# Optimization experiments

Measured on AMD Instinct MI355X. Metric: run time of the kernel, lower is better.

Reference implementation:

```python
import jax, jax.numpy as jnp
import numpy as np

EMBED_DIM = 512
N_HEADS = 8
HEAD_DIM = EMBED_DIM // N_HEADS
N_BINS = 512
MAX_BIN = 256
SCALE = 1.0 / np.sqrt(HEAD_DIM)


def _l2norm(x):
    # manifold.project onto unit sphere along last dim
    n = jnp.sqrt(jnp.sum(x * x, axis=-1, keepdims=True))
    return x / jnp.maximum(n, 1e-12)


def setup_inputs() -> dict:
    rng = jax.random.key(0)
    ks = jax.random.split(rng, 13)
    B, N, D = 1, 2048, EMBED_DIM
    s = 1.0 / np.sqrt(D)
    cen = jax.random.normal(ks[12], (N_BINS, HEAD_DIM), dtype=jnp.float32)
    return {
        "query": jax.random.normal(ks[0], (B, N, D), dtype=jnp.float32),
        "key": jax.random.normal(ks[1], (B, N, D), dtype=jnp.float32),
        "value": jax.random.normal(ks[2], (B, N, D), dtype=jnp.float32),
        "Wq": jax.random.normal(ks[3], (D, D), dtype=jnp.float32) * s,
        "bq": jax.random.normal(ks[4], (D,), dtype=jnp.float32) * s,
        "Wk": jax.random.normal(ks[5], (D, D), dtype=jnp.float32) * s,
        "bk": jax.random.normal(ks[6], (D,), dtype=jnp.float32) * s,
        "Wv": jax.random.normal(ks[7], (D, D), dtype=jnp.float32) * s,
        "bv": jax.random.normal(ks[8], (D,), dtype=jnp.float32) * s,
        "Wo": jax.random.normal(ks[9], (D, D), dtype=jnp.float32) * s,
        "bo": jax.random.normal(ks[10], (D,), dtype=jnp.float32) * s,
        "centroids": _l2norm(cen),  # unit bin centroids of dim head_dim
    }


def reference(query, key, value, Wq, bq, Wk, bk, Wv, bv, Wo, bo, centroids):
    B, Nq, D = query.shape
    Nk = key.shape[1]
    H, hd = N_HEADS, HEAD_DIM

    def split(x):  # [B,N,D] -> [B,H,N,hd]
        return x.reshape(B, -1, H, hd).transpose(0, 2, 1, 3)

    q = split(query @ Wq.T + bq)
    k = split(key @ Wk.T + bk)
    v = split(value @ Wv.T + bv)

    # manifold.project (sphere): attention uses the projected q/k, raw v
    qn = _l2norm(q)
    kn = _l2norm(k)

    # DavisCache: nearest-centroid bin id  [B,H,N]
    qb = jnp.argmax(jnp.einsum('bhnd,cd->bhnc', qn, centroids), axis=-1).astype(jnp.int32)
    kb = jnp.argmax(jnp.einsum('bhnd,cd->bhnc', kn, centroids), axis=-1).astype(jnp.int32)

    # neighboring_bins(qb, radius=1) on a ring: kb in {qb-1, qb, qb+1} mod N_BINS
    diff = (qb[..., :, None] - kb[..., None, :]) % N_BINS  # [B,H,Nq,Nk]
    neigh = (diff <= 1) | (diff >= N_BINS - 1)

    # truncate to first MAX_BIN selected keys (index order), as in the loop
    rank = jnp.cumsum(neigh.astype(jnp.int32), axis=-1)  # inclusive count
    sel = neigh & (rank <= MAX_BIN)
    # fallback: empty neighbor set -> all keys, then truncated to first MAX_BIN
    fallback = (jnp.arange(Nk, dtype=jnp.int32) < MAX_BIN)
    mask = jnp.where(neigh.any(axis=-1, keepdims=True), sel, fallback)

    scores = jnp.einsum('bhqd,bhkd->bhqk', qn, kn) * jnp.float32(SCALE)
    scores = jnp.where(mask, scores, jnp.float32(-1e30))
    attn = jax.nn.softmax(scores, axis=-1)  # dropout=0.0 (eval)
    out = jnp.einsum('bhqk,bhkd->bhqd', attn, v)

    out = out.transpose(0, 2, 1, 3).reshape(B, Nq, D)
    return out @ Wo.T + bo
```

## Files before the change

### kernel.cpp

```cpp
#include <hip/hip_runtime.h>
#include <hip/hip_bf16.h>

#define NTOK 2048
#define EMBED 512
#define NHEADS 8
#define HD 64
#define NBINS 512
#define MAXSEL 256

typedef unsigned short u16;
typedef unsigned int u32;

__device__ __forceinline__ float lof(u32 u){ return __uint_as_float(u << 16); }
__device__ __forceinline__ float hif(u32 u){ return __uint_as_float(u & 0xffff0000u); }
__device__ __forceinline__ float bf2f(u16 u){ return __uint_as_float(((u32)u) << 16); }
__device__ __forceinline__ u16 f2b(float f){
    __hip_bfloat16 h = __float2bfloat16(f);
    return *(u16*)&h;
}
__device__ __forceinline__ u32 pack2(float lo, float hi){
    return (u32)f2b(lo) | ((u32)f2b(hi) << 16);
}
__device__ __forceinline__ void fma8(const float* x, u32 ux, u32 uy, u32 uz, u32 uw, float& a){
    a += x[0]*lof(ux) + x[1]*hif(ux) + x[2]*lof(uy) + x[3]*hif(uy)
       + x[4]*lof(uz) + x[5]*hif(uz) + x[6]*lof(uw) + x[7]*hif(uw);
}

__device__ __forceinline__ u32 sniffp(const void* p){
    const u16* s = (const u16*)p;
    float m = 0.f;
    #pragma unroll
    for (int k=0; k<64; k++) m = fmaxf(m, fabsf(bf2f(s[2*k])));
    return (m > 100.f) ? 1u : 0u;
}

__device__ __forceinline__ void ub2(const uint4& u, float4& f0, float4& f1){
    f0 = make_float4(lof(u.x), hif(u.x), lof(u.y), hif(u.y));
    f1 = make_float4(lof(u.z), hif(u.z), lof(u.w), hif(u.w));
}

__device__ __forceinline__ void fma16x2(const float* xp,
    const float4& a0, const float4& a1, const float4& a2, const float4& a3,
    const float4& b0, const float4& b1, const float4& b2, const float4& b3,
    float& A, float& B)
{
    float4 x0 = *(const float4*)(xp);
    float4 x1 = *(const float4*)(xp+4);
    float4 x2 = *(const float4*)(xp+8);
    float4 x3 = *(const float4*)(xp+12);
    A += x0.x*a0.x; A += x0.y*a0.y; A += x0.z*a0.z; A += x0.w*a0.w;
    A += x1.x*a1.x; A += x1.y*a1.y; A += x1.z*a1.z; A += x1.w*a1.w;
    A += x2.x*a2.x; A += x2.y*a2.y; A += x2.z*a2.z; A += x2.w*a2.w;
    A += x3.x*a3.x; A += x3.y*a3.y; A += x3.z*a3.z; A += x3.w*a3.w;
    B += x0.x*b0.x; B += x0.y*b0.y; B += x0.z*b0.z; B += x0.w*b0.w;
    B += x1.x*b1.x; B += x1.y*b1.y; B += x1.z*b1.z; B += x1.w*b1.w;
    B += x2.x*b2.x; B += x2.y*b2.y; B += x2.z*b2.z; B += x2.w*b2.w;
    B += x3.x*b3.x; B += x3.y*b3.y; B += x3.z*b3.z; B += x3.w*b3.w;
}

__global__ __launch_bounds__(256) void projqkv_kernel(
    const void* __restrict__ Xq, const void* __restrict__ Xk, const void* __restrict__ Xv,
    const void* __restrict__ Wq, const void* __restrict__ bq,
    const void* __restrict__ Wk, const void* __restrict__ bk,
    const void* __restrict__ Wv, const void* __restrict__ bv,
    const void* __restrict__ cen,
    void* __restrict__ outQ,
    u16* __restrict__ Kb, u16* __restrict__ Vb,
    u16* __restrict__ qbin, u16* __restrict__ kbin)
{
    int which = blockIdx.y;
    const void *X, *W, *Bb;
    if (which==0){ X=Xq; W=Wq; Bb=bq; }
    else if (which==1){ X=Xk; W=Wk; Bb=bk; }
    else { X=Xv; W=Wv; Bb=bv; }
    u32 fx = sniffp(X), fw = sniffp(W), fb = sniffp(Bb);
    int r0 = blockIdx.x * 8;
    int t = threadIdx.x;

    __shared__ __align__(16) float ubuf[4608];
    __shared__ __align__(16) float ps[64*68];
    __shared__ float nrm2[64][4];
    __shared__ float invn[64];
    __shared__ float bvl[64][8];
    __shared__ int   bil[64][8];

    float* xstage = ps;
    for (int i=t; i<1024; i+=256){
        int row = i>>7, c4 = i&127;
        float4 v;
        if (!fx){
            const u32* xp = (const u32*)((const u16*)X + (size_t)(r0+row)*EMBED);
            u32 a = xp[c4*2], b = xp[c4*2+1];
            v = make_float4(lof(a), hif(a), lof(b), hif(b));
        } else {
            v = ((const float4*)((const float*)X + (size_t)(r0+row)*EMBED))[c4];
        }
        *(float4*)(xstage + row*516 + c4*4) = v;
    }
    __syncthreads();

    float acc2[8][2];
    #pragma unroll
    for (int r=0;r<8;r++){ acc2[r][0]=0.f; acc2[r][1]=0.f; }

    if (fw){
        const float* w1 = (const float*)W + (size_t)t*EMBED;
        const float* w2 = (const float*)W + (size_t)(t+256)*EMBED;
        float4 pa0 = *(const float4*)(w1+ 0), pa1 = *(const float4*)(w1+ 4),
               pa2 = *(const float4*)(w1+ 8), pa3 = *(const float4*)(w1+12);
        float4 pb0 = *(const float4*)(w2+ 0), pb1 = *(const float4*)(w2+ 4),
               pb2 = *(const float4*)(w2+ 8), pb3 = *(const float4*)(w2+12);
        #pragma unroll 1
        for (int k0=0; k0<512; k0+=32){
            float4 qa0 = *(const float4*)(w1+k0+16), qa1 = *(const float4*)(w1+k0+20),
                   qa2 = *(const float4*)(w1+k0+24), qa3 = *(const float4*)(w1+k0+28);
            float4 qb0 = *(const float4*)(w2+k0+16), qb1 = *(const float4*)(w2+k0+20),
                   qb2 = *(const float4*)(w2+k0+24), qb3 = *(const float4*)(w2+k0+28);
            #pragma unroll
            for (int r=0;r<8;r++)
                fma16x2(xstage + r*516 + k0, pa0,pa1,pa2,pa3, pb0,pb1,pb2,pb3,
                        acc2[r][0], acc2[r][1]);
            if (k0+32 < 512){
                pa0 = *(const float4*)(w1+k0+32); pa1 = *(const float4*)(w1+k0+36);
                pa2 = *(const float4*)(w1+k0+40); pa3 = *(const float4*)(w1+k0+44);
                pb0 = *(const float4*)(w2+k0+32); pb1 = *(const float4*)(w2+k0+36);
                pb2 = *(const float4*)(w2+k0+40); pb3 = *(const float4*)(w2+k0+44);
            }
            #pragma unroll
            for (int r=0;r<8;r++)
                fma16x2(xstage + r*516 + k0+16, qa0,qa1,qa2,qa3, qb0,qb1,qb2,qb3,
                        acc2[r][0], acc2[r][1]);
        }
    } else {
        const uint4* w1 = (const uint4*)((const u16*)W + (size_t)t*EMBED);
        const uint4* w2 = (const uint4*)((const u16*)W + (size_t)(t+256)*EMBED);
        uint4 pa0 = w1[0], pa1 = w1[1], pb0 = w2[0], pb1 = w2[1];
        #pragma unroll 1
        for (int k0=0; k0<512; k0+=32){
            int u = k0>>3;
            uint4 qa0 = w1[u+2], qa1 = w1[u+3], qb0 = w2[u+2], qb1 = w2[u+3];
            float4 a0,a1,a2,a3,b0,b1,b2,b3;
            ub2(pa0,a0,a1); ub2(pa1,a2,a3); ub2(pb0,b0,b1); ub2(pb1,b2,b3);
            #pragma unroll
            for (int r=0;r<8;r++)
                fma16x2(xstage + r*516 + k0, a0,a1,a2,a3, b0,b1,b2,b3,
                        acc2[r][0], acc2[r][1]);
            if (k0+32 < 512){ pa0 = w1[u+4]; pa1 = w1[u+5]; pb0 = w2[u+4]; pb1 = w2[u+5]; }
            ub2(qa0,a0,a1); ub2(qa1,a2,a3); ub2(qb0,b0,b1); ub2(qb1,b2,b3);
            #pragma unroll
            for (int r=0;r<8;r++)
                fma16x2(xstage + r*516 + k0+16, a0,a1,a2,a3, b0,b1,b2,b3,
                        acc2[r][0], acc2[r][1]);
        }
    }
    __syncthreads();
    {
        float b0 = fb ? ((const float*)Bb)[t]     : bf2f(((const u16*)Bb)[t]);
        float b1 = fb ? ((const float*)Bb)[t+256] : bf2f(((const u16*)Bb)[t+256]);
        int h0 = t>>6, c0 = t&63, h1 = (t+256)>>6, c1 = (t+256)&63;
        #pragma unroll
        for (int r=0;r<8;r++){
            ps[(r*8+h0)*68 + c0] = acc2[r][0]+b0;
            ps[(r*8+h1)*68 + c1] = acc2[r][1]+b1;
        }
    }
    __syncthreads();

    if (which == 2){
        int hr = t>>2, q4 = t&3;
        int row = hr>>3, head = hr&7;
        const float* src = ps + hr*68 + q4*16;
        u16* dst = Vb + (size_t)(r0+row)*EMBED + head*64 + q4*16;
        #pragma unroll
        for (int j8=0;j8<2;j8++){
            uint4 v;
            v.x = pack2(src[j8*8+0],src[j8*8+1]); v.y = pack2(src[j8*8+2],src[j8*8+3]);
            v.z = pack2(src[j8*8+4],src[j8*8+5]); v.w = pack2(src[j8*8+6],src[j8*8+7]);
            ((uint4*)dst)[j8] = v;
        }
        return;
    }

    u32 fc = sniffp(cen);
    int rg = t>>3, cg = t&7;
    float best[2] = {-3.4e38f,-3.4e38f};
    int   bidx[2] = {0,0};
    float cpre[16];
    #pragma unroll
    for (int it=0; it<16; it++){
        int e = t + it*256, j = e>>6, k = e&63;
        cpre[it] = fc ? ((const float*)cen)[(size_t)j*HD + k]
                      : bf2f(((const u16*)cen)[(size_t)j*HD + k]);
    }
    for (int tt=0; tt<8; tt++){
        __syncthreads();
        #pragma unroll
        for (int it=0; it<16; it++){
            int e = t + it*256, j = e>>6, k = e&63;
            ubuf[k*68 + j] = cpre[it];
        }
        if (tt < 7){
            #pragma unroll
            for (int it=0; it<16; it++){
                int e = t + it*256, j = e>>6, k = e&63;
                int gj = (tt+1)*64 + j;
                cpre[it] = fc ? ((const float*)cen)[(size_t)gj*HD + k]
                              : bf2f(((const u16*)cen)[(size_t)gj*HD + k]);
            }
        }
        __syncthreads();
        float acc[2][8];
        #pragma unroll
        for (int j=0;j<2;j++)
            #pragma unroll
            for (int c=0;c<8;c++) acc[j][c]=0.f;
        const float* pr0 = ps + (2*rg)*68;
        const float* pr1 = pr0 + 68;
        #pragma unroll 1
        for (int k4=0;k4<64;k4+=4){
            float4 ra = *(const float4*)(pr0 + k4);
            float4 rb = *(const float4*)(pr1 + k4);
            const float* cbase = ubuf + k4*68 + cg*8;
            #define SCANK(OFF, AX, BX) { \
                const float4* cp = (const float4*)(cbase + (OFF)); \
                float4 c0 = cp[0], c1 = cp[1]; \
                acc[0][0]+=(AX)*c0.x; acc[0][1]+=(AX)*c0.y; acc[0][2]+=(AX)*c0.z; acc[0][3]+=(AX)*c0.w; \
                acc[0][4]+=(AX)*c1.x; acc[0][5]+=(AX)*c1.y; acc[0][6]+=(AX)*c1.z; acc[0][7]+=(AX)*c1.w; \
                acc[1][0]+=(BX)*c0.x; acc[1][1]+=(BX)*c0.y; acc[1][2]+=(BX)*c0.z; acc[1][3]+=(BX)*c0.w; \
                acc[1][4]+=(BX)*c1.x; acc[1][5]+=(BX)*c1.y; acc[1][6]+=(BX)*c1.z; acc[1][7]+=(BX)*c1.w; }
            SCANK(0,   ra.x, rb.x)
            SCANK(68,  ra.y, rb.y)
            SCANK(136, ra.z, rb.z)
            SCANK(204, ra.w, rb.w)
            #undef SCANK
        }
        #pragma unroll
        for (int j=0;j<2;j++){
            #pragma unroll
            for (int c=0;c<8;c++){
                int gi = tt*64 + cg*8 + c;
                if (acc[j][c] > best[j]){ best[j]=acc[j][c]; bidx[j]=gi; }
            }
        }
    }
    bvl[2*rg  ][cg]=best[0]; bil[2*rg  ][cg]=bidx[0];
    bvl[2*rg+1][cg]=best[1]; bil[2*rg+1][cg]=bidx[1];
    {
        int hr = t>>2, q4 = t&3;
        const float* src = ps + hr*68 + q4*16;
        float ss=0.f;
        #pragma unroll
        for (int d=0;d<16;d++) ss += src[d]*src[d];
        nrm2[hr][q4]=ss;
    }
    __syncthreads();
    if (t < 64){
        int hr = t;
        invn[hr] = 1.f / fmaxf(sqrtf(nrm2[hr][0]+nrm2[hr][1]+nrm2[hr][2]+nrm2[hr][3]), 1e-12f);
        float bv = bvl[hr][0]; int bi = bil[hr][0];
        #pragma unroll
        for (int g=1; g<8; g++){
            float ov = bvl[hr][g]; int oi = bil[hr][g];
            if (ov > bv || (ov == bv && oi < bi)){ bv = ov; bi = oi; }
        }
        u16* bins = (which==0) ? qbin : kbin;
        int token = r0 + (hr>>3), head = hr&7;
        bins[head*NTOK + token] = (u16)bi;
    }
    __syncthreads();
    {
        int hr = t>>2, q4 = t&3;
        float inv = invn[hr];
        const float* src = ps + hr*68 + q4*16;
        int row = hr>>3, head = hr&7;
        size_t off = (size_t)(r0+row)*EMBED + head*64 + q4*16;
        if (which == 1){
            u16* dst = Kb + off;
            #pragma unroll
            for (int j8=0;j8<2;j8++){
                uint4 v;
                v.x = pack2(src[j8*8+0]*inv, src[j8*8+1]*inv);
                v.y = pack2(src[j8*8+2]*inv, src[j8*8+3]*inv);
                v.z = pack2(src[j8*8+4]*inv, src[j8*8+5]*inv);
                v.w = pack2(src[j8*8+6]*inv, src[j8*8+7]*inv);
                ((uint4*)dst)[j8] = v;
            }
        } else if (!fx){
            u16* dst = (u16*)outQ + off;
            #pragma unroll
            for (int j8=0;j8<2;j8++){
                uint4 v;
                v.x = pack2(src[j8*8+0]*inv, src[j8*8+1]*inv);
                v.y = pack2(src[j8*8+2]*inv, src[j8*8+3]*inv);
                v.z = pack2(src[j8*8+4]*inv, src[j8*8+5]*inv);
                v.w = pack2(src[j8*8+6]*inv, src[j8*8+7]*inv);
                ((uint4*)dst)[j8] = v;
            }
        } else {
            float* dst = (float*)outQ + off;
            #pragma unroll
            for (int j4=0;j4<4;j4++){
                float4 v = make_float4(src[j4*4+0]*inv, src[j4*4+1]*inv,
                                       src[j4*4+2]*inv, src[j4*4+3]*inv);
                ((float4*)dst)[j4] = v;
            }
        }
    }
}

__global__ __launch_bounds__(256) void attn_kernel(
    const void* __restrict__ query,
    const u16* __restrict__ Kb, const u16* __restrict__ Vb,
    const u16* __restrict__ qbin, const u16* __restrict__ kbin,
    void* __restrict__ out)
{
    u32 fq = sniffp(query);
    int q = blockIdx.x, t = threadIdx.x;
    int wave = t>>6, lane = t&63;
    __shared__ float qs[512];
    __shared__ float sc[4][256];
    __shared__ u16   sel[4][256];

    if (!fq){
        u32 u = ((const u32*)out)[(size_t)q*256 + t];
        qs[2*t] = lof(u); qs[2*t+1] = hif(u);
    } else {
        float2 f = ((const float2*)out)[(size_t)q*256 + t];
        qs[2*t] = f.x; qs[2*t+1] = f.y;
    }
    __syncthreads();

    for (int hh=0; hh<2; hh++){
        int h = wave*2 + hh;
        int myqb = qbin[h*NTOK + q];
        const uint4* kbp = (const uint4*)(kbin + h*NTOK + lane*32);
        u32 fl = 0;
        #pragma unroll
        for (int w4=0; w4<4; w4++){
            uint4 kw = kbp[w4];
            u32 arr[4] = {kw.x, kw.y, kw.z, kw.w};
            #pragma unroll
            for (int e=0;e<4;e++){
                int b0 = (int)(arr[e] & 0xffff), b1 = (int)(arr[e] >> 16);
                int d0 = (myqb - b0) & (NBINS-1), d1 = (myqb - b1) & (NBINS-1);
                if (d0 <= 1 || d0 >= NBINS-1) fl |= 1u << (w4*8 + e*2);
                if (d1 <= 1 || d1 >= NBINS-1) fl |= 1u << (w4*8 + e*2 + 1);
            }
        }
        int cnt = __popc(fl);
        int sum = cnt;
        #pragma unroll
        for (int off=1; off<64; off<<=1){
            int v = __shfl_up(sum, off, 64);
            if (lane >= off) sum += v;
        }
        int total = __shfl(sum, 63, 64);
        int r = sum - cnt;
        if (total){
            u32 f2 = fl;
            while (f2){
                int j = __ffs(f2) - 1; f2 &= f2 - 1;
                if (r < MAXSEL) sel[wave][r] = (u16)(lane*32 + j);
                r++;
            }
        } else {
            #pragma unroll
            for (int kq=0;kq<4;kq++) sel[wave][lane*4+kq] = (u16)(lane*4+kq);
        }
        int L = total ? min(total, MAXSEL) : MAXSEL;
        __asm__ volatile("s_waitcnt lgkmcnt(0)" ::: "memory");
        const float* qh = qs + h*64;

        if (L <= 64){
            int kkey = 0;
            float s = -3.4e38f;
            if (lane < L){
                kkey = sel[wave][lane];
                const uint4* kr = (const uint4*)(Kb + (size_t)kkey*EMBED + h*64);
                float acc = 0.f;
                #pragma unroll
                for (int p=0;p<8;p++){ uint4 u = kr[p]; fma8(qh+p*8, u.x,u.y,u.z,u.w, acc); }
                s = acc * 0.125f;
            }
            float mloc = s;
            #pragma unroll
            for (int off=32; off; off>>=1) mloc = fmaxf(mloc, __shfl_xor(mloc, off, 64));
            float e = (lane < L) ? __expf(s - mloc) : 0.f;
            float ssum = e;
            #pragma unroll
            for (int off=32; off; off>>=1) ssum += __shfl_xor(ssum, off, 64);
            float inv = 1.f / fmaxf(ssum, 1e-37f);
            const u16* vb = Vb + h*64 + lane;
            float acc = 0.f;
            int j = 0;
            for (; j+4<=L; j+=4){
                float e0 = __shfl(e, j,   64), e1 = __shfl(e, j+1, 64);
                float e2 = __shfl(e, j+2, 64), e3 = __shfl(e, j+3, 64);
                int   k0 = __shfl(kkey, j,   64), k1 = __shfl(kkey, j+1, 64);
                int   k2 = __shfl(kkey, j+2, 64), k3 = __shfl(kkey, j+3, 64);
                float v0 = bf2f(vb[(size_t)k0*EMBED]);
                float v1 = bf2f(vb[(size_t)k1*EMBED]);
                float v2 = bf2f(vb[(size_t)k2*EMBED]);
                float v3 = bf2f(vb[(size_t)k3*EMBED]);
                acc += e0*v0; acc += e1*v1; acc += e2*v2; acc += e3*v3;
            }
            for (; j<L; j++){
                float ej = __shfl(e, j, 64);
                int   kj = __shfl(kkey, j, 64);
                acc += ej * bf2f(vb[(size_t)kj*EMBED]);
            }
            float o = acc * inv;
            if (!fq) ((u16*)out)[(size_t)q*EMBED + h*64 + lane] = f2b(o);
            else     ((float*)out)[(size_t)q*EMBED + h*64 + lane] = o;
        } else {
            float mloc = -3.4e38f;
            for (int jj=lane; jj<L; jj+=64){
                int kkey = sel[wave][jj];
                const uint4* kr = (const uint4*)(Kb + (size_t)kkey*EMBED + h*64);
                float acc = 0.f;
                #pragma unroll
                for (int p=0;p<8;p++){ uint4 u = kr[p]; fma8(qh+p*8, u.x,u.y,u.z,u.w, acc); }
                float s = acc * 0.125f;
                sc[wave][jj] = s;
                mloc = fmaxf(mloc, s);
            }
            #pragma unroll
            for (int off=32; off; off>>=1) mloc = fmaxf(mloc, __shfl_xor(mloc, off, 64));
            float ssum = 0.f;
            for (int jj=lane; jj<L; jj+=64){
                float e = __expf(sc[wave][jj] - mloc);
                sc[wave][jj] = e; ssum += e;
            }
            #pragma unroll
            for (int off=32; off; off>>=1) ssum += __shfl_xor(ssum, off, 64);
            float inv = 1.f / fmaxf(ssum, 1e-37f);
            __asm__ volatile("s_waitcnt lgkmcnt(0)" ::: "memory");
            float acc = 0.f;
            for (int j=0; j<L; j++){
                int kkey = sel[wave][j];
                acc += sc[wave][j] * bf2f(Vb[(size_t)kkey*EMBED + h*64 + lane]);
            }
            float o = acc * inv;
            if (!fq) ((u16*)out)[(size_t)q*EMBED + h*64 + lane] = f2b(o);
            else     ((float*)out)[(size_t)q*EMBED + h*64 + lane] = o;
        }
    }
}

__global__ __launch_bounds__(256) void oproj_kernel(
    void* __restrict__ out, const void* __restrict__ Wo, const void* __restrict__ bo)
{
    u32 fq = sniffp(out);
    u32 fw = sniffp(Wo), fb = sniffp(bo);
    int r0 = blockIdx.x * 8;
    int t = threadIdx.x;
    __shared__ __align__(16) float xst[8*516];

    for (int i=t; i<1024; i+=256){
        int row = i>>7, c4 = i&127;
        float4 v;
        if (!fq){
            const u32* xp = (const u32*)((const u16*)out + (size_t)(r0+row)*EMBED);
            u32 a = xp[c4*2], b = xp[c4*2+1];
            v = make_float4(lof(a), hif(a), lof(b), hif(b));
        } else {
            v = ((const float4*)((const float*)out + (size_t)(r0+row)*EMBED))[c4];
        }
        *(float4*)(xst + row*516 + c4*4) = v;
    }
    __syncthreads();

    float acc2[8][2];
    #pragma unroll
    for (int r=0;r<8;r++){ acc2[r][0]=0.f; acc2[r][1]=0.f; }

    if (fw){
        const float* w1 = (const float*)Wo + (size_t)t*EMBED;
        const float* w2 = (const float*)Wo + (size_t)(t+256)*EMBED;
        float4 pa0 = *(const float4*)(w1+ 0), pa1 = *(const float4*)(w1+ 4),
               pa2 = *(const float4*)(w1+ 8), pa3 = *(const float4*)(w1+12);
        float4 pb0 = *(const float4*)(w2+ 0), pb1 = *(const float4*)(w2+ 4),
               pb2 = *(const float4*)(w2+ 8), pb3 = *(const float4*)(w2+12);
        #pragma unroll 1
        for (int k0=0; k0<512; k0+=32){
            float4 qa0 = *(const float4*)(w1+k0+16), qa1 = *(const float4*)(w1+k0+20),
                   qa2 = *(const float4*)(w1+k0+24), qa3 = *(const float4*)(w1+k0+28);
            float4 qb0 = *(const float4*)(w2+k0+16), qb1 = *(const float4*)(w2+k0+20),
                   qb2 = *(const float4*)(w2+k0+24), qb3 = *(const float4*)(w2+k0+28);
            #pragma unroll
            for (int r=0;r<8;r++)
                fma16x2(xst + r*516 + k0, pa0,pa1,pa2,pa3, pb0,pb1,pb2,pb3,
                        acc2[r][0], acc2[r][1]);
            if (k0+32 < 512){
                pa0 = *(const float4*)(w1+k0+32); pa1 = *(const float4*)(w1+k0+36);
                pa2 = *(const float4*)(w1+k0+40); pa3 = *(const float4*)(w1+k0+44);
                pb0 = *(const float4*)(w2+k0+32); pb1 = *(const float4*)(w2+k0+36);
                pb2 = *(const float4*)(w2+k0+40); pb3 = *(const float4*)(w2+k0+44);
            }
            #pragma unroll
            for (int r=0;r<8;r++)
                fma16x2(xst + r*516 + k0+16, qa0,qa1,qa2,qa3, qb0,qb1,qb2,qb3,
                        acc2[r][0], acc2[r][1]);
        }
    } else {
        const uint4* w1 = (const uint4*)((const u16*)Wo + (size_t)t*EMBED);
        const uint4* w2 = (const uint4*)((const u16*)Wo + (size_t)(t+256)*EMBED);
        uint4 pa0 = w1[0], pa1 = w1[1], pb0 = w2[0], pb1 = w2[1];
        #pragma unroll 1
        for (int k0=0; k0<512; k0+=32){
            int u = k0>>3;
            uint4 qa0 = w1[u+2], qa1 = w1[u+3], qb0 = w2[u+2], qb1 = w2[u+3];
            float4 a0,a1,a2,a3,b0,b1,b2,b3;
            ub2(pa0,a0,a1); ub2(pa1,a2,a3); ub2(pb0,b0,b1); ub2(pb1,b2,b3);
            #pragma unroll
            for (int r=0;r<8;r++)
                fma16x2(xst + r*516 + k0, a0,a1,a2,a3, b0,b1,b2,b3,
                        acc2[r][0], acc2[r][1]);
            if (k0+32 < 512){ pa0 = w1[u+4]; pa1 = w1[u+5]; pb0 = w2[u+4]; pb1 = w2[u+5]; }
            ub2(qa0,a0,a1); ub2(qa1,a2,a3); ub2(qb0,b0,b1); ub2(qb1,b2,b3);
            #pragma unroll
            for (int r=0;r<8;r++)
                fma16x2(xst + r*516 + k0+16, a0,a1,a2,a3, b0,b1,b2,b3,
                        acc2[r][0], acc2[r][1]);
        }
    }
    float b0 = fb ? ((const float*)bo)[t]     : bf2f(((const u16*)bo)[t]);
    float b1 = fb ? ((const float*)bo)[t+256] : bf2f(((const u16*)bo)[t+256]);
    if (!fq){
        u16* o = (u16*)out;
        #pragma unroll
        for (int r=0;r<8;r++){
            o[(size_t)(r0+r)*EMBED + t]       = f2b(acc2[r][0]+b0);
            o[(size_t)(r0+r)*EMBED + t + 256] = f2b(acc2[r][1]+b1);
        }
    } else {
        float* o = (float*)out;
        #pragma unroll
        for (int r=0;r<8;r++){
            o[(size_t)(r0+r)*EMBED + t]       = acc2[r][0]+b0;
            o[(size_t)(r0+r)*EMBED + t + 256] = acc2[r][1]+b1;
        }
    }
}

extern "C" void kernel_launch(void* const* d_in, const int* in_sizes, int n_in,
                              void* d_out, int out_size, void* d_ws, size_t ws_size,
                              hipStream_t stream)
{
    const void* query = d_in[0];
    const void* key   = d_in[1];
    const void* value = d_in[2];
    const void* Wq = d_in[3];
    const void* bq = d_in[4];
    const void* Wk = d_in[5];
    const void* bk = d_in[6];
    const void* Wv = d_in[7];
    const void* bv = d_in[8];
    const void* Wo = d_in[9];
    const void* bo = d_in[10];
    const void* cen = d_in[11];

    char* ws = (char*)d_ws;
    u16* qbin = (u16*)ws;
    u16* kbin = (u16*)(ws + 32768);
    u16* Kb   = (u16*)(ws + 65536);
    u16* Vb   = (u16*)(ws + 65536 + (size_t)2*1024*1024);

    projqkv_kernel<<<dim3(256,3), 256, 0, stream>>>(query,key,value,Wq,bq,Wk,bk,Wv,bv,cen,
                                                    d_out,Kb,Vb,qbin,kbin);
    attn_kernel<<<2048, 256, 0, stream>>>(query,Kb,Vb,qbin,kbin,d_out);
    oproj_kernel<<<256, 256, 0, stream>>>(d_out,Wo,bo);
}
```

Measured before the change: 277.7 us.

## Split K across thread halves so each thread accumulates four projection columns

The QKV projection GEMM is reorganised so that each thread computes four output columns over half of the K dimension, with the two halves of the block splitting K. The upper half writes its partial sums to a shared buffer, and the lower half adds them together with the bias. Each staged x vector read from LDS now feeds four weight rows instead of two, which cuts LDS traffic per FMA. The cost is an extra shared-memory reduction, a sync, and more accumulator registers.

```diff
diff --git a/kernel.cpp b/kernel.cpp
--- a/kernel.cpp
+++ b/kernel.cpp
@@ -37,6 +37,14 @@
 __device__ __forceinline__ void ub2(const uint4& u, float4& f0, float4& f1){
     f0 = make_float4(lof(u.x), hif(u.x), lof(u.y), hif(u.y));
     f1 = make_float4(lof(u.z), hif(u.z), lof(u.w), hif(u.w));
+}
+
+__device__ __forceinline__ float dot8(const float4& x0, const float4& x1,
+                                      const float4& a0, const float4& a1){
+    float s;
+    s  = x0.x*a0.x; s += x0.y*a0.y; s += x0.z*a0.z; s += x0.w*a0.w;
+    s += x1.x*a1.x; s += x1.y*a1.y; s += x1.z*a1.z; s += x1.w*a1.w;
+    return s;
 }
 
 __device__ __forceinline__ void fma16x2(const float* xp,
@@ -99,69 +107,98 @@
     }
     __syncthreads();
 
-    float acc2[8][2];
+    int tp = t & 127;
+    int kh = t >> 7;
+    int kbase = kh << 8;
+
+    float acc4[8][4];
     #pragma unroll
-    for (int r=0;r<8;r++){ acc2[r][0]=0.f; acc2[r][1]=0.f; }
+    for (int r=0;r<8;r++){ acc4[r][0]=0.f; acc4[r][1]=0.f; acc4[r][2]=0.f; acc4[r][3]=0.f; }
 
     if (fw){
-        const float* w1 = (const float*)W + (size_t)t*EMBED;
-        const float* w2 = (const float*)W + (size_t)(t+256)*EMBED;
-        float4 pa0 = *(const float4*)(w1+ 0), pa1 = *(const float4*)(w1+ 4),
-               pa2 = *(const float4*)(w1+ 8), pa3 = *(const float4*)(w1+12);
-        float4 pb0 = *(const float4*)(w2+ 0), pb1 = *(const float4*)(w2+ 4),
-               pb2 = *(const float4*)(w2+ 8), pb3 = *(const float4*)(w2+12);
+        const float* w0 = (const float*)W + (size_t)(tp      )*EMBED + kbase;
+        const float* w1 = (const float*)W + (size_t)(tp + 128)*EMBED + kbase;
+        const float* w2 = (const float*)W + (size_t)(tp + 256)*EMBED + kbase;
+        const float* w3 = (const float*)W + (size_t)(tp + 384)*EMBED + kbase;
+        float4 a00 = *(const float4*)(w0+0), a01 = *(const float4*)(w0+4);
+        float4 a10 = *(const float4*)(w1+0), a11 = *(const float4*)(w1+4);
+        float4 a20 = *(const float4*)(w2+0), a21 = *(const float4*)(w2+4);
+        float4 a30 = *(const float4*)(w3+0), a31 = *(const float4*)(w3+4);
         #pragma unroll 1
-        for (int k0=0; k0<512; k0+=32){
-            float4 qa0 = *(const float4*)(w1+k0+16), qa1 = *(const float4*)(w1+k0+20),
-                   qa2 = *(const float4*)(w1+k0+24), qa3 = *(const float4*)(w1+k0+28);
-            float4 qb0 = *(const float4*)(w2+k0+16), qb1 = *(const float4*)(w2+k0+20),
-                   qb2 = *(const float4*)(w2+k0+24), qb3 = *(const float4*)(w2+k0+28);
-            #pragma unroll
-            for (int r=0;r<8;r++)
-                fma16x2(xstage + r*516 + k0, pa0,pa1,pa2,pa3, pb0,pb1,pb2,pb3,
-                        acc2[r][0], acc2[r][1]);
-            if (k0+32 < 512){
-                pa0 = *(const float4*)(w1+k0+32); pa1 = *(const float4*)(w1+k0+36);
-                pa2 = *(const float4*)(w1+k0+40); pa3 = *(const float4*)(w1+k0+44);
-                pb0 = *(const float4*)(w2+k0+32); pb1 = *(const float4*)(w2+k0+36);
-                pb2 = *(const float4*)(w2+k0+40); pb3 = *(const float4*)(w2+k0+44);
-            }
-            #pragma unroll
-            for (int r=0;r<8;r++)
-                fma16x2(xstage + r*516 + k0+16, qa0,qa1,qa2,qa3, qb0,qb1,qb2,qb3,
-                        acc2[r][0], acc2[r][1]);
+        for (int k0=0; k0<256; k0+=8){
+            float4 b00,b01,b10,b11,b20,b21,b30,b31;
+            if (k0+8 < 256){
+                b00 = *(const float4*)(w0+k0+8);  b01 = *(const float4*)(w0+k0+12);
+                b10 = *(const float4*)(w1+k0+8);  b11 = *(const float4*)(w1+k0+12);
+                b20 = *(const float4*)(w2+k0+8);  b21 = *(const float4*)(w2+k0+12);
+                b30 = *(const float4*)(w3+k0+8);  b31 = *(const float4*)(w3+k0+12);
+            }
+            #pragma unroll
+            for (int r=0;r<8;r++){
+                const float* xp = xstage + r*516 + kbase + k0;
+                float4 x0 = *(const float4*)(xp);
+                float4 x1 = *(const float4*)(xp+4);
+                acc4[r][0] += dot8(x0,x1,a00,a01);
+                acc4[r][1] += dot8(x0,x1,a10,a11);
+                acc4[r][2] += dot8(x0,x1,a20,a21);
+                acc4[r][3] += dot8(x0,x1,a30,a31);
+            }
+            if (k0+8 < 256){
+                a00=b00; a01=b01; a10=b10; a11=b11;
+                a20=b20; a21=b21; a30=b30; a31=b31;
+            }
         }
     } else {
-        const uint4* w1 = (const uint4*)((const u16*)W + (size_t)t*EMBED);
-        const uint4* w2 = (const uint4*)((const u16*)W + (size_t)(t+256)*EMBED);
-        uint4 pa0 = w1[0], pa1 = w1[1], pb0 = w2[0], pb1 = w2[1];
+        const uint4* w0 = (const uint4*)((const u16*)W + (size_t)(tp      )*EMBED + kbase);
+        const uint4* w1 = (const uint4*)((const u16*)W + (size_t)(tp + 128)*EMBED + kbase);
+        const uint4* w2 = (const uint4*)((const u16*)W + (size_t)(tp + 256)*EMBED + kbase);
+        const uint4* w3 = (const uint4*)((const u16*)W + (size_t)(tp + 384)*EMBED + kbase);
+        uint4 u0 = w0[0], u1 = w1[0], u2 = w2[0], u3 = w3[0];
         #pragma unroll 1
-        for (int k0=0; k0<512; k0+=32){
-            int u = k0>>3;
-            uint4 qa0 = w1[u+2], qa1 = w1[u+3], qb0 = w2[u+2], qb1 = w2[u+3];
-            float4 a0,a1,a2,a3,b0,b1,b2,b3;
-            ub2(pa0,a0,a1); ub2(pa1,a2,a3); ub2(pb0,b0,b1); ub2(pb1,b2,b3);
-            #pragma unroll
-            for (int r=0;r<8;r++)
-                fma16x2(xstage + r*516 + k0, a0,a1,a2,a3, b0,b1,b2,b3,
-                        acc2[r][0], acc2[r][1]);
-            if (k0+32 < 512){ pa0 = w1[u+4]; pa1 = w1[u+5]; pb0 = w2[u+4]; pb1 = w2[u+5]; }
-            ub2(qa0,a0,a1); ub2(qa1,a2,a3); ub2(qb0,b0,b1); ub2(qb1,b2,b3);
-            #pragma unroll
-            for (int r=0;r<8;r++)
-                fma16x2(xstage + r*516 + k0+16, a0,a1,a2,a3, b0,b1,b2,b3,
-                        acc2[r][0], acc2[r][1]);
+        for (int k0=0; k0<256; k0+=8){
+            int i8 = k0>>3;
+            uint4 v0,v1,v2,v3;
+            if (k0+8 < 256){ v0 = w0[i8+1]; v1 = w1[i8+1]; v2 = w2[i8+1]; v3 = w3[i8+1]; }
+            float4 a00,a01,a10,a11,a20,a21,a30,a31;
+            ub2(u0,a00,a01); ub2(u1,a10,a11); ub2(u2,a20,a21); ub2(u3,a30,a31);
+            #pragma unroll
+            for (int r=0;r<8;r++){
+                const float* xp = xstage + r*516 + kbase + k0;
+                float4 x0 = *(const float4*)(xp);
+                float4 x1 = *(const float4*)(xp+4);
+                acc4[r][0] += dot8(x0,x1,a00,a01);
+                acc4[r][1] += dot8(x0,x1,a10,a11);
+                acc4[r][2] += dot8(x0,x1,a20,a21);
+                acc4[r][3] += dot8(x0,x1,a30,a31);
+            }
+            if (k0+8 < 256){ u0=v0; u1=v1; u2=v2; u3=v3; }
+        }
+    }
+    if (kh){
+        #pragma unroll
+        for (int r=0;r<8;r++){
+            #pragma unroll
+            for (int c=0;c<4;c++)
+                ubuf[(r*4+c)*132 + tp] = acc4[r][c];
         }
     }
     __syncthreads();
-    {
-        float b0 = fb ? ((const float*)Bb)[t]     : bf2f(((const u16*)Bb)[t]);
-        float b1 = fb ? ((const float*)Bb)[t+256] : bf2f(((const u16*)Bb)[t+256]);
-        int h0 = t>>6, c0 = t&63, h1 = (t+256)>>6, c1 = (t+256)&63;
+    if (!kh){
+        float bc0, bc1, bc2, bc3;
+        if (fb){
+            const float* bp = (const float*)Bb;
+            bc0=bp[tp]; bc1=bp[tp+128]; bc2=bp[tp+256]; bc3=bp[tp+384];
+        } else {
+            const u16* bp = (const u16*)Bb;
+            bc0=bf2f(bp[tp]); bc1=bf2f(bp[tp+128]); bc2=bf2f(bp[tp+256]); bc3=bf2f(bp[tp+384]);
+        }
+        int cw = tp & 63, hb = tp >> 6;
         #pragma unroll
         for (int r=0;r<8;r++){
-            ps[(r*8+h0)*68 + c0] = acc2[r][0]+b0;
-            ps[(r*8+h1)*68 + c1] = acc2[r][1]+b1;
+            ps[(r*8 + hb    )*68 + cw] = (acc4[r][0] + ubuf[(r*4+0)*132 + tp]) + bc0;
+            ps[(r*8 + hb + 2)*68 + cw] = (acc4[r][1] + ubuf[(r*4+1)*132 + tp]) + bc1;
+            ps[(r*8 + hb + 4)*68 + cw] = (acc4[r][2] + ubuf[(r*4+2)*132 + tp]) + bc2;
+            ps[(r*8 + hb + 6)*68 + cw] = (acc4[r][3] + ubuf[(r*4+3)*132 + tp]) + bc3;
         }
     }
     __syncthreads();
```

After: 294.6 us. 1.06x slower.
